# Optimization experiments

Measured on AMD Instinct MI355X. Metric: run time of the kernel, lower is better.

The kernel has to match this reference:

```python
import jax, jax.numpy as jnp
import numpy as np
from jax import lax

B, D, H, W = 1, 8, 64, 64
C, WS, NH = 192, 8, 6
N = WS ** 3          # 512 tokens per window
HD = C // NH         # 32
CONV_SCALE = 0.01
EPS = 1e-5
DN = ('NCDHW', 'OIDHW', 'NCDHW')


def _make_rpi():
    c = np.stack(np.meshgrid(np.arange(WS), np.arange(WS), np.arange(WS), indexing='ij')).reshape(3, -1)
    rel = (c[:, :, None] - c[:, None, :]).transpose(1, 2, 0) + (WS - 1)  # [N,N,3]
    idx = rel[..., 0] * (2 * WS - 1) ** 2 + rel[..., 1] * (2 * WS - 1) + rel[..., 2]
    return jnp.asarray(idx, dtype=jnp.int32)


def _ln(x, g, b):
    m = x.mean(-1, keepdims=True)
    v = jnp.mean((x - m) ** 2, -1, keepdims=True)
    return (x - m) * lax.rsqrt(v + EPS) * g + b


def setup_inputs() -> dict:
    key = jax.random.key(0)
    ks = jax.random.split(key, 16)
    s = 0.02
    inp = {
        'x': jax.random.normal(ks[0], (B, D * H * W, C), jnp.float32),
        'norm1_g': jnp.ones((C,), jnp.float32), 'norm1_b': jnp.zeros((C,), jnp.float32),
        'qkv_w': jax.random.normal(ks[1], (3 * C, C), jnp.float32) * s,
        'qkv_b': jnp.zeros((3 * C,), jnp.float32),
        'rpb_table': jax.random.normal(ks[2], (3375, NH), jnp.float32) * s,
        'proj_w': jax.random.normal(ks[3], (C, C), jnp.float32) * s,
        'proj_b': jnp.zeros((C,), jnp.float32),
        'conv1_w': jax.random.normal(ks[4], (C // 3, C, 3, 3, 3), jnp.float32) * s,
        'conv1_b': jnp.zeros((C // 3,), jnp.float32),
        'conv2_w': jax.random.normal(ks[5], (C, C // 3, 3, 3, 3), jnp.float32) * s,
        'conv2_b': jnp.zeros((C,), jnp.float32),
        'ca1_w': jax.random.normal(ks[6], (6, C), jnp.float32) * s,
        'ca1_b': jnp.zeros((6,), jnp.float32),
        'ca2_w': jax.random.normal(ks[7], (C, 6), jnp.float32) * s,
        'ca2_b': jnp.zeros((C,), jnp.float32),
        'norm2_g': jnp.ones((C,), jnp.float32), 'norm2_b': jnp.zeros((C,), jnp.float32),
        'fc1_w': jax.random.normal(ks[8], (4 * C, C), jnp.float32) * s,
        'fc1_b': jnp.zeros((4 * C,), jnp.float32),
        'fc2_w': jax.random.normal(ks[9], (C, 4 * C), jnp.float32) * s,
        'fc2_b': jnp.zeros((C,), jnp.float32),
        'rpi': _make_rpi(),
    }
    return inp


def reference(x, norm1_g, norm1_b, qkv_w, qkv_b, rpb_table, proj_w, proj_b,
              conv1_w, conv1_b, conv2_w, conv2_b, ca1_w, ca1_b, ca2_w, ca2_b,
              norm2_g, norm2_b, fc1_w, fc1_b, fc2_w, fc2_b, rpi):
    shortcut = x
    xn = _ln(x, norm1_g, norm1_b)                      # [B, L, C]
    x5 = xn.reshape(B, D, H, W, C)

    # ---- CAB3D conv branch (conv3x3 -> gelu -> conv3x3 -> channel attention)
    xc = jnp.transpose(x5, (0, 4, 1, 2, 3))            # NCDHW
    h = lax.conv_general_dilated(xc, conv1_w, (1, 1, 1), 'SAME', dimension_numbers=DN)
    h = jax.nn.gelu(h + conv1_b[None, :, None, None, None], approximate=False)
    h = lax.conv_general_dilated(h, conv2_w, (1, 1, 1), 'SAME', dimension_numbers=DN)
    h = h + conv2_b[None, :, None, None, None]
    pooled = h.mean(axis=(2, 3, 4))                    # [B, C] global avg pool
    a = jax.nn.relu(pooled @ ca1_w.T + ca1_b)
    a = jax.nn.sigmoid(a @ ca2_w.T + ca2_b)            # [B, C]
    conv_x = (h * a[:, :, None, None, None])
    conv_x = jnp.transpose(conv_x, (0, 2, 3, 4, 1)).reshape(B, D * H * W, C)

    # ---- window partition (shift_size forced to 0 since min(res)==window_size)
    xw = x5.reshape(B, D // WS, WS, H // WS, WS, W // WS, WS, C)
    xw = jnp.transpose(xw, (0, 1, 3, 5, 2, 4, 6, 7)).reshape(-1, N, C)  # [nW, N, C]

    # ---- window attention with relative position bias
    qkv = (xw @ qkv_w.T + qkv_b).reshape(-1, N, 3, NH, HD)
    q = jnp.transpose(qkv[:, :, 0], (0, 2, 1, 3)) * (HD ** -0.5)  # [nW, h, N, d]
    k = jnp.transpose(qkv[:, :, 1], (0, 2, 1, 3))
    v = jnp.transpose(qkv[:, :, 2], (0, 2, 1, 3))
    attn = jnp.einsum('whnd,whmd->whnm', q, k)
    bias = rpb_table[rpi]                              # [N, N, h]
    attn = attn + jnp.transpose(bias, (2, 0, 1))[None]
    attn = jax.nn.softmax(attn, axis=-1)
    out = jnp.einsum('whnm,whmd->whnd', attn, v)
    out = jnp.transpose(out, (0, 2, 1, 3)).reshape(-1, N, C)
    out = out @ proj_w.T + proj_b

    # ---- window reverse
    out = out.reshape(B, D // WS, H // WS, W // WS, WS, WS, WS, C)
    out = jnp.transpose(out, (0, 1, 4, 2, 5, 3, 6, 7)).reshape(B, D * H * W, C)

    x2 = shortcut + out + conv_x * CONV_SCALE
    xm = _ln(x2, norm2_g, norm2_b)
    xm = jax.nn.gelu(xm @ fc1_w.T + fc1_b, approximate=False) @ fc2_w.T + fc2_b
    return x2 + xm
```

## Files before the change

### kernel.cpp

```cpp
#include <hip/hip_runtime.h>
#include <hip/hip_bf16.h>

#define LTOK  32768
#define CDIM  192
#define DD_   8
#define HH_   64
#define WW_   64
#define NHEAD 6
#define HDIM  32
#define NWIN  64
#define NTOKW 512
#define C3    64
#define FCH   768

#define OFF_XN     0u
#define OFF_QH     6291456u
#define OFF_KH     9437184u
#define OFF_VH     12582912u
#define OFF_Y      15728640u
#define OFF_YBF    18874368u
#define OFF_H1     22020096u
#define OFF_H2     24117248u
#define OFF_PART   30408704u
#define OFF_AMASK  30457856u
#define OFF_BIAST  30458048u
#define OFF_W1T    32030912u
#define OFF_W2T    32362688u
#define OFF_QKVT   32694464u
#define OFF_PROJT  32805056u
#define OFF_FC1T   32841920u
#define OFF_FC2T   32989376u

typedef __attribute__((ext_vector_type(8)))  short short8v;
typedef __attribute__((ext_vector_type(16))) float f32x16;

union FragU { short8v v; unsigned u[4]; };

__device__ __forceinline__ float gelu_exact(float x) {
    return 0.5f * x * (1.0f + erff(x * 0.70710678118654752f));
}

__device__ __forceinline__ unsigned short bf16bits(float x) {
    union { __hip_bfloat16 b; unsigned short u; } cv;
    cv.b = __float2bfloat16(x);
    return cv.u;
}

__global__ __launch_bounds__(256) void k_ln(const float* __restrict__ in,
                                            const float* __restrict__ g,
                                            const float* __restrict__ b,
                                            float* __restrict__ out,
                                            __hip_bfloat16* __restrict__ obf) {
    int wv = threadIdx.x >> 6, lane = threadIdx.x & 63;
    int t = blockIdx.x * 4 + wv;
    const float* row = in + (size_t)t * CDIM;
    float x0 = row[lane], x1 = row[lane + 64], x2 = row[lane + 128];
    float s = x0 + x1 + x2;
    for (int o = 32; o; o >>= 1) s += __shfl_xor(s, o);
    float m = s * (1.0f / 192.0f);
    float d0 = x0 - m, d1 = x1 - m, d2 = x2 - m;
    float vv = d0 * d0 + d1 * d1 + d2 * d2;
    for (int o = 32; o; o >>= 1) vv += __shfl_xor(vv, o);
    float inv = rsqrtf(vv * (1.0f / 192.0f) + 1e-5f);
    size_t base = (size_t)t * CDIM;
    float y0 = d0 * inv * g[lane]       + b[lane];
    float y1 = d1 * inv * g[lane + 64]  + b[lane + 64];
    float y2 = d2 * inv * g[lane + 128] + b[lane + 128];
    if (out) {
        out[base + lane]       = y0;
        out[base + lane + 64]  = y1;
        out[base + lane + 128] = y2;
    }
    if (obf) {
        obf[base + lane]       = __float2bfloat16(y0);
        obf[base + lane + 64]  = __float2bfloat16(y1);
        obf[base + lane + 128] = __float2bfloat16(y2);
    }
}

__global__ void k_cast(const float* __restrict__ in, __hip_bfloat16* __restrict__ out, int n) {
    int i = blockIdx.x * 256 + threadIdx.x;
    if (i < n) out[i] = __float2bfloat16(in[i]);
}

__global__ void k_wp1(const float* __restrict__ w, __hip_bfloat16* __restrict__ wp) {
    int i = blockIdx.x * 256 + threadIdx.x;
    if (i >= 331776) return;
    int j = i & 7, oc = (i >> 3) & 63, h = (i >> 9) & 1;
    int cg = (i >> 10) % 12, kk = i / 12288;
    int c = cg * 16 + h * 8 + j;
    wp[i] = __float2bfloat16(w[((size_t)oc * 192 + c) * 27 + kk]);
}
__global__ void k_wp2(const float* __restrict__ w, __hip_bfloat16* __restrict__ wp) {
    int i = blockIdx.x * 256 + threadIdx.x;
    if (i >= 331776) return;
    int j = i & 7, oc = (i >> 3) % 192;
    int h = (i / 1536) & 1, cg = (i / 3072) & 3, kk = i / 12288;
    int c = cg * 16 + h * 8 + j;
    wp[i] = __float2bfloat16(w[((size_t)oc * 64 + c) * 27 + kk]);
}

__global__ __launch_bounds__(256) void k_bias(const int* __restrict__ rpi,
                                              const float* __restrict__ rpb,
                                              float* __restrict__ biasT) {
    __shared__ int idxl[64][64];
    int tid = threadIdx.x;
    int n0 = (blockIdx.x >> 3) * 64, m0 = (blockIdx.x & 7) * 64;
    for (int it = 0; it < 16; it++) {
        int e = it * 256 + tid;
        int ln_ = e >> 6, lm = e & 63;
        idxl[ln_][lm] = rpi[(size_t)(n0 + ln_) * NTOKW + m0 + lm];
    }
    __syncthreads();
    for (int it = 0; it < 16; it++) {
        int e = it * 256 + tid;
        int lm = e >> 6, ln_ = e & 63;
        int id = idxl[ln_][lm];
        #pragma unroll
        for (int h = 0; h < NHEAD; h++)
            biasT[(size_t)h * NTOKW * NTOKW + (size_t)(m0 + lm) * NTOKW + n0 + ln_] =
                rpb[id * NHEAD + h];
    }
}

__global__ __launch_bounds__(256) void k_conv1m(const __hip_bfloat16* __restrict__ xnbf,
                                                const __hip_bfloat16* __restrict__ w1p,
                                                const float* __restrict__ b1,
                                                __hip_bfloat16* __restrict__ h1bf) {
    __shared__ __align__(16) char lds[66 * 384];
    int tid = threadIdx.x;
    int wv = tid >> 6, lane = tid & 63;
    int wr = wv >> 1, wc = wv & 1;
    int half = lane >> 5, l31 = lane & 31;
    int row = blockIdx.x;
    int d = row >> 6, hh = row & 63;

    if (tid < 48) {
        float4 z = {0.f, 0.f, 0.f, 0.f};
        char* p = lds + ((tid < 24) ? tid * 16 : 65 * 384 + (tid - 24) * 16);
        *(float4*)p = z;
    }

    f32x16 acc;
    #pragma unroll
    for (int r = 0; r < 16; r++) acc[r] = 0.f;

    for (int kd = -1; kd <= 1; kd++) {
        int dd = d + kd;
        if (dd < 0 || dd >= DD_) continue;
        for (int kh = -1; kh <= 1; kh++) {
            int h2 = hh + kh;
            if (h2 < 0 || h2 >= HH_) continue;
            const short* src = (const short*)xnbf + ((size_t)((dd << 12) | (h2 << 6))) * CDIM;
            __syncthreads();
            #pragma unroll
            for (int it = 0; it < 6; it++) {
                int e16 = it * 256 + tid;
                int tok = e16 / 24, cb = (e16 % 24) * 16;
                short8v vdat = *(const short8v*)(src + e16 * 8);
                int lrow = tok + 1;
                *(short8v*)(lds + lrow * 384 + (cb ^ ((lrow & 7) << 4))) = vdat;
            }
            __syncthreads();
            #pragma unroll
            for (int kw = -1; kw <= 1; kw++) {
                int kk = (kd + 1) * 9 + (kh + 1) * 3 + (kw + 1);
                int atok = 32 * wr + l31 + kw + 1;
                int akey = (atok & 7) << 4;
                const char* abase = lds + atok * 384;
                const short* wbase = (const short*)w1p + (kk * 24 + half) * 512 + (32 * wc + l31) * 8;
                #pragma unroll
                for (int cg = 0; cg < 12; cg++) {
                    short8v af = *(const short8v*)(abase + ((cg * 32 + half * 16) ^ akey));
                    short8v bf = *(const short8v*)(wbase + cg * 1024);
                    acc = __builtin_amdgcn_mfma_f32_32x32x16_bf16(af, bf, acc, 0, 0, 0);
                }
            }
        }
    }
    int oc = 32 * wc + l31;
    float bb = b1[oc];
    int t0 = row * 64;
    #pragma unroll
    for (int r = 0; r < 16; r++) {
        int tok = 32 * wr + (r & 3) + 8 * (r >> 2) + 4 * half;
        h1bf[(size_t)(t0 + tok) * C3 + oc] = __float2bfloat16(gelu_exact(acc[r] + bb));
    }
}

__global__ __launch_bounds__(384) void k_conv2m(const __hip_bfloat16* __restrict__ h1bf,
                                                const __hip_bfloat16* __restrict__ w2p,
                                                const float* __restrict__ b2,
                                                float* __restrict__ h2) {
    __shared__ __align__(16) char lds[34 * 128];
    int tid = threadIdx.x;
    int wv = tid >> 6, lane = tid & 63;
    int half = lane >> 5, l31 = lane & 31;
    int row = blockIdx.x >> 1, hr = blockIdx.x & 1;
    int d = row >> 6, hh = row & 63;

    f32x16 acc;
    #pragma unroll
    for (int r = 0; r < 16; r++) acc[r] = 0.f;

    for (int kd = -1; kd <= 1; kd++) {
        int dd = d + kd;
        if (dd < 0 || dd >= DD_) continue;
        for (int kh = -1; kh <= 1; kh++) {
            int h2r = hh + kh;
            if (h2r < 0 || h2r >= HH_) continue;
            __syncthreads();
            if (tid < 272) {
                int ti = tid >> 3, cb = (tid & 7) * 16;
                int w = hr * 32 + ti - 1;
                short8v vdat = {0, 0, 0, 0, 0, 0, 0, 0};
                if (w >= 0 && w < 64)
                    vdat = *(const short8v*)((const short*)h1bf +
                           (size_t)((dd << 12) | (h2r << 6) | w) * C3 + cb / 2);
                *(short8v*)(lds + ti * 128 + (cb ^ ((ti & 7) << 4))) = vdat;
            }
            __syncthreads();
            #pragma unroll
            for (int kw = -1; kw <= 1; kw++) {
                int kk = (kd + 1) * 9 + (kh + 1) * 3 + (kw + 1);
                int atok = l31 + kw + 1;
                int akey = (atok & 7) << 4;
                const char* abase = lds + atok * 128;
                const short* wbase = (const short*)w2p + (kk * 8 + half) * 1536 + (wv * 32 + l31) * 8;
                #pragma unroll
                for (int cg = 0; cg < 4; cg++) {
                    short8v af = *(const short8v*)(abase + ((cg * 32 + half * 16) ^ akey));
                    short8v bf = *(const short8v*)(wbase + cg * 3072);
                    acc = __builtin_amdgcn_mfma_f32_32x32x16_bf16(af, bf, acc, 0, 0, 0);
                }
            }
        }
    }
    int oc = wv * 32 + l31;
    float bb = b2[oc];
    int t0 = row * 64 + hr * 32;
    #pragma unroll
    for (int r = 0; r < 16; r++) {
        int tok = (r & 3) + 8 * (r >> 2) + 4 * half;
        h2[(size_t)(t0 + tok) * CDIM + oc] = acc[r] + bb;
    }
}

__global__ __launch_bounds__(192) void k_pool(const float* __restrict__ h2,
                                              float* __restrict__ part) {
    int c = threadIdx.x, b = blockIdx.x;
    float s = 0.f;
    for (int i = 0; i < 128; i++) s += h2[(size_t)(b * 128 + i) * CDIM + c];
    part[b * CDIM + c] = s;
}

__global__ __launch_bounds__(192) void k_ca(const float* __restrict__ part,
                                            const float* __restrict__ ca1w,
                                            const float* __restrict__ ca1b,
                                            const float* __restrict__ ca2w,
                                            const float* __restrict__ ca2b,
                                            float* __restrict__ amask) {
    __shared__ float pooled[CDIM];
    __shared__ float hid[6];
    int c = threadIdx.x;
    float s = 0.f;
    for (int b = 0; b < 256; b++) s += part[b * CDIM + c];
    pooled[c] = s * (1.0f / 32768.0f);
    __syncthreads();
    if (c < 6) {
        float a = ca1b[c];
        for (int j = 0; j < CDIM; j++) a += ca1w[c * CDIM + j] * pooled[j];
        hid[c] = fmaxf(a, 0.f);
    }
    __syncthreads();
    float a = ca2b[c];
    for (int j = 0; j < 6; j++) a += ca2w[c * 6 + j] * hid[j];
    amask[c] = 1.0f / (1.0f + expf(-a));
}

__global__ __launch_bounds__(64) void k_qkvm(const __hip_bfloat16* __restrict__ xnbf,
                                             const __hip_bfloat16* __restrict__ qwb,
                                             const float* __restrict__ qkvb,
                                             __hip_bfloat16* __restrict__ q,
                                             __hip_bfloat16* __restrict__ k,
                                             __hip_bfloat16* __restrict__ v) {
    __shared__ __align__(16) char xlds[32 * 384];
    __shared__ float tb[32][33];
    int lane = threadIdx.x;
    int half = lane >> 5, l31 = lane & 31;
    int t0 = blockIdx.x * 32;
    int wi = t0 >> 9;
    int wh_ = wi >> 3, ww_ = wi & 7;

    #pragma unroll
    for (int it = 0; it < 12; it++) {
        int e16 = it * 64 + lane;
        int tok = e16 / 24, cb = (e16 % 24) * 16;
        int n = (t0 + tok) & 511;
        int nd = n >> 6, nh = (n >> 3) & 7, nw = n & 7;
        int torig = (nd << 12) | ((wh_ * 8 + nh) << 6) | (ww_ * 8 + nw);
        short8v vdat = *(const short8v*)((const short*)xnbf + (size_t)torig * CDIM + (e16 % 24) * 8);
        *(short8v*)(xlds + tok * 384 + (cb ^ ((tok & 7) << 4))) = vdat;
    }
    __syncthreads();

    int akey = (l31 & 7) << 4;
    const char* xbase = xlds + l31 * 384;

    for (int ti = 0; ti < 18; ti++) {
        f32x16 acc;
        #pragma unroll
        for (int r = 0; r < 16; r++) acc[r] = 0.f;
        const short* wbase = (const short*)qwb + (size_t)(ti * 32 + l31) * CDIM + half * 8;
        #pragma unroll
        for (int cg = 0; cg < 12; cg++) {
            short8v bf = *(const short8v*)(xbase + ((cg * 32 + half * 16) ^ akey));
            short8v af = *(const short8v*)(wbase + cg * 16);
            acc = __builtin_amdgcn_mfma_f32_32x32x16_bf16(af, bf, acc, 0, 0, 0);
        }
        #pragma unroll
        for (int r = 0; r < 16; r++) {
            int dl = (r & 3) + 8 * (r >> 2) + 4 * half;
            tb[l31][dl] = acc[r];
        }
        asm volatile("s_waitcnt lgkmcnt(0)" ::: "memory");
        __builtin_amdgcn_sched_barrier(0);
        int tok = lane >> 1, d0 = (lane & 1) * 16;
        int type = ti / 6, head = ti % 6;
        float scale = (type == 0) ? 0.17677669529663687f : 1.0f;
        int n = (t0 + tok) & 511;
        __hip_bfloat16* dst = (type == 0 ? q : (type == 1 ? k : v)) +
                              ((size_t)((wi * NHEAD + head) * NTOKW + n)) * HDIM + d0;
        const float* bp = qkvb + ti * 32 + d0;
        short8v o0, o1;
        #pragma unroll
        for (int i = 0; i < 8; i++)
            o0[i] = (short)bf16bits((tb[tok][d0 + i] + bp[i]) * scale);
        #pragma unroll
        for (int i = 0; i < 8; i++)
            o1[i] = (short)bf16bits((tb[tok][d0 + 8 + i] + bp[8 + i]) * scale);
        *(short8v*)((short*)dst) = o0;
        *(short8v*)((short*)dst + 8) = o1;
        asm volatile("s_waitcnt lgkmcnt(0)" ::: "memory");
        __builtin_amdgcn_sched_barrier(0);
    }
}

__global__ __launch_bounds__(256) void k_attn(const __hip_bfloat16* __restrict__ qh,
                                              const __hip_bfloat16* __restrict__ kh,
                                              const __hip_bfloat16* __restrict__ vh,
                                              const float* __restrict__ biasT,
                                              __hip_bfloat16* __restrict__ outbf) {
    __shared__ float ot[4][32][33];
    int wv = threadIdx.x >> 6, lane = threadIdx.x & 63;
    int tile = blockIdx.x * 4 + wv;
    int qt = tile & 15, wh = tile >> 4;
    int head = wh % NHEAD, wi = wh / NHEAD;
    int qb = qt * 32;
    int h = lane >> 5, ln31 = lane & 31;

    const unsigned short* qp = (const unsigned short*)qh + ((size_t)wh * NTOKW + qb + ln31) * HDIM;
    short8v qf0 = *(const short8v*)(qp + 8 * h);
    short8v qf1 = *(const short8v*)(qp + 16 + 8 * h);
    const unsigned short* kbase = (const unsigned short*)kh + (size_t)wh * NTOKW * HDIM;
    const unsigned short* vbase = (const unsigned short*)vh + (size_t)wh * NTOKW * HDIM;
    const float* bbase = biasT + (size_t)head * NTOKW * NTOKW + qb + ln31;

    f32x16 O;
    #pragma unroll
    for (int r = 0; r < 16; r++) O[r] = 0.f;
    float m = -1e30f, l = 0.f;

    for (int kb = 0; kb < NTOKW; kb += 32) {
        const unsigned short* kp = kbase + (size_t)(kb + ln31) * HDIM;
        short8v kf0 = *(const short8v*)(kp + 8 * h);
        short8v kf1 = *(const short8v*)(kp + 16 + 8 * h);
        f32x16 S;
        #pragma unroll
        for (int r = 0; r < 16; r++) S[r] = 0.f;
        S = __builtin_amdgcn_mfma_f32_32x32x16_bf16(kf0, qf0, S, 0, 0, 0);
        S = __builtin_amdgcn_mfma_f32_32x32x16_bf16(kf1, qf1, S, 0, 0, 0);

        float s[16];
        #pragma unroll
        for (int r = 0; r < 16; r++) {
            int key = (r & 3) + 8 * (r >> 2) + 4 * h;
            s[r] = S[r] + bbase[(size_t)(kb + key) * NTOKW];
        }
        float cm = s[0];
        #pragma unroll
        for (int r = 1; r < 16; r++) cm = fmaxf(cm, s[r]);
        cm = fmaxf(cm, __shfl_xor(cm, 32));
        float mn = fmaxf(m, cm);
        float scale = __expf(m - mn);
        float e[16]; float cs = 0.f;
        #pragma unroll
        for (int r = 0; r < 16; r++) { e[r] = __expf(s[r] - mn); cs += e[r]; }
        cs += __shfl_xor(cs, 32);
        l = l * scale + cs;
        m = mn;
        #pragma unroll
        for (int r = 0; r < 16; r++) O[r] *= scale;

        unsigned P[8], Qx[8];
        #pragma unroll
        for (int i = 0; i < 8; i++)
            P[i] = (unsigned)bf16bits(e[2 * i]) | ((unsigned)bf16bits(e[2 * i + 1]) << 16);
        #pragma unroll
        for (int i = 0; i < 8; i++) Qx[i] = __shfl_xor(P[i], 32);

        FragU p0, p1;
        p0.u[0] = h ? Qx[2] : P[0];  p0.u[1] = h ? Qx[3] : P[1];
        p0.u[2] = h ? P[2]  : Qx[0]; p0.u[3] = h ? P[3]  : Qx[1];
        p1.u[0] = h ? Qx[6] : P[4];  p1.u[1] = h ? Qx[7] : P[5];
        p1.u[2] = h ? P[6]  : Qx[4]; p1.u[3] = h ? P[7]  : Qx[5];

        const unsigned short* vp0 = vbase + (size_t)(kb + 8 * h) * HDIM + ln31;
        const unsigned short* vp1 = vbase + (size_t)(kb + 16 + 8 * h) * HDIM + ln31;
        short8v vf0, vf1;
        #pragma unroll
        for (int i = 0; i < 8; i++) {
            vf0[i] = (short)vp0[i * HDIM];
            vf1[i] = (short)vp1[i * HDIM];
        }
        O = __builtin_amdgcn_mfma_f32_32x32x16_bf16(vf0, p0.v, O, 0, 0, 0);
        O = __builtin_amdgcn_mfma_f32_32x32x16_bf16(vf1, p1.v, O, 0, 0, 0);
    }

    float invl = 1.0f / l;
    #pragma unroll
    for (int r = 0; r < 16; r++) {
        int d = (r & 3) + 8 * (r >> 2) + 4 * h;
        ot[wv][ln31][d] = O[r] * invl;
    }
    __syncthreads();
    int t2 = lane >> 1, c0 = (lane & 1) * 16;
    short* outp = (short*)outbf + ((size_t)(wi * NTOKW + qb + t2)) * CDIM + head * HDIM + c0;
    short8v s0, s1;
    #pragma unroll
    for (int i = 0; i < 8; i++) s0[i] = (short)bf16bits(ot[wv][t2][c0 + i]);
    #pragma unroll
    for (int i = 0; i < 8; i++) s1[i] = (short)bf16bits(ot[wv][t2][c0 + 8 + i]);
    *(short8v*)outp = s0;
    *(short8v*)(outp + 8) = s1;
}

__global__ __launch_bounds__(64) void k_projm(const __hip_bfloat16* __restrict__ attnbf,
                                              const __hip_bfloat16* __restrict__ pwb,
                                              const float* __restrict__ pb,
                                              const float* __restrict__ x,
                                              const float* __restrict__ h2,
                                              const float* __restrict__ amask,
                                              float* __restrict__ x2) {
    __shared__ __align__(16) char alds[32 * 384];
    __shared__ float tb[32][33];
    int lane = threadIdx.x;
    int half = lane >> 5, l31 = lane & 31;
    int t0 = blockIdx.x * 32;
    int wi = t0 >> 9;
    int wh_ = wi >> 3, ww_ = wi & 7;

    const short* src = (const short*)attnbf + (size_t)t0 * CDIM;
    #pragma unroll
    for (int it = 0; it < 12; it++) {
        int e16 = it * 64 + lane;
        int tok = e16 / 24, cb = (e16 % 24) * 16;
        short8v vdat = *(const short8v*)(src + e16 * 8);
        *(short8v*)(alds + tok * 384 + (cb ^ ((tok & 7) << 4))) = vdat;
    }
    __syncthreads();

    int akey = (l31 & 7) << 4;
    const char* abase = alds + l31 * 384;

    for (int ot = 0; ot < 6; ot++) {
        f32x16 acc;
        #pragma unroll
        for (int r = 0; r < 16; r++) acc[r] = 0.f;
        const short* wbase = (const short*)pwb + (size_t)(ot * 32 + l31) * CDIM + half * 8;
        #pragma unroll
        for (int cg = 0; cg < 12; cg++) {
            short8v bf = *(const short8v*)(abase + ((cg * 32 + half * 16) ^ akey));
            short8v af = *(const short8v*)(wbase + cg * 16);
            acc = __builtin_amdgcn_mfma_f32_32x32x16_bf16(af, bf, acc, 0, 0, 0);
        }
        #pragma unroll
        for (int r = 0; r < 16; r++) {
            int oc = (r & 3) + 8 * (r >> 2) + 4 * half;
            tb[l31][oc] = acc[r];
        }
        asm volatile("s_waitcnt lgkmcnt(0)" ::: "memory");
        __builtin_amdgcn_sched_barrier(0);
        int tok = lane >> 1, c0 = (lane & 1) * 16;
        int n = (t0 + tok) & 511;
        int nd = n >> 6, nh = (n >> 3) & 7, nw = n & 7;
        int t = (nd << 12) | ((wh_ * 8 + nh) << 6) | (ww_ * 8 + nw);
        size_t idx = (size_t)t * CDIM + ot * 32 + c0;
        const float* bp = pb + ot * 32 + c0;
        const float* ap = amask + ot * 32 + c0;
        #pragma unroll
        for (int i = 0; i < 16; i++)
            x2[idx + i] = x[idx + i] + tb[tok][c0 + i] + bp[i] + 0.01f * h2[idx + i] * ap[i];
        asm volatile("s_waitcnt lgkmcnt(0)" ::: "memory");
        __builtin_amdgcn_sched_barrier(0);
    }
}

__global__ __launch_bounds__(64) void k_mlpm(const __hip_bfloat16* __restrict__ ybf,
                                             const __hip_bfloat16* __restrict__ w1b,
                                             const float* __restrict__ b1,
                                             const __hip_bfloat16* __restrict__ w2b,
                                             const float* __restrict__ b2,
                                             float* __restrict__ out) {
    __shared__ __align__(16) char ylds[32 * 384];
    int lane = threadIdx.x;
    int half = lane >> 5, l31 = lane & 31;
    int t0 = blockIdx.x * 32;

    const short* src = (const short*)ybf + (size_t)t0 * CDIM;
    #pragma unroll
    for (int it = 0; it < 12; it++) {
        int e16 = it * 64 + lane;
        int tok = e16 / 24, cb = (e16 % 24) * 16;
        short8v vdat = *(const short8v*)(src + e16 * 8);
        *(short8v*)(ylds + tok * 384 + (cb ^ ((tok & 7) << 4))) = vdat;
    }
    __syncthreads();

    int akey = (l31 & 7) << 4;
    const char* ybase = ylds + l31 * 384;

    f32x16 oacc[6];
    #pragma unroll
    for (int ot = 0; ot < 6; ot++)
        #pragma unroll
        for (int r = 0; r < 16; r++) oacc[ot][r] = 0.f;

    for (int hc = 0; hc < 24; hc++) {
        f32x16 hacc;
        #pragma unroll
        for (int r = 0; r < 16; r++) hacc[r] = 0.f;
        const short* w1base = (const short*)w1b + (size_t)(hc * 32 + l31) * CDIM + half * 8;
        #pragma unroll
        for (int cg = 0; cg < 12; cg++) {
            short8v bf = *(const short8v*)(ybase + ((cg * 32 + half * 16) ^ akey));
            short8v af = *(const short8v*)(w1base + cg * 16);
            hacc = __builtin_amdgcn_mfma_f32_32x32x16_bf16(af, bf, hacc, 0, 0, 0);
        }
        float e[16];
        #pragma unroll
        for (int r = 0; r < 16; r++) {
            int hid = (r & 3) + 8 * (r >> 2) + 4 * half;
            e[r] = gelu_exact(hacc[r] + b1[hc * 32 + hid]);
        }
        unsigned P[8], Qx[8];
        #pragma unroll
        for (int i = 0; i < 8; i++)
            P[i] = (unsigned)bf16bits(e[2 * i]) | ((unsigned)bf16bits(e[2 * i + 1]) << 16);
        #pragma unroll
        for (int i = 0; i < 8; i++) Qx[i] = __shfl_xor(P[i], 32);
        FragU p0, p1;
        p0.u[0] = half ? Qx[2] : P[0];  p0.u[1] = half ? Qx[3] : P[1];
        p0.u[2] = half ? P[2]  : Qx[0]; p0.u[3] = half ? P[3]  : Qx[1];
        p1.u[0] = half ? Qx[6] : P[4];  p1.u[1] = half ? Qx[7] : P[5];
        p1.u[2] = half ? P[6]  : Qx[4]; p1.u[3] = half ? P[7]  : Qx[5];

        const short* w2base = (const short*)w2b + (size_t)l31 * FCH + hc * 32 + half * 8;
        #pragma unroll
        for (int ot = 0; ot < 6; ot++) {
            short8v a0 = *(const short8v*)(w2base + (size_t)ot * 32 * FCH);
            short8v a1 = *(const short8v*)(w2base + (size_t)ot * 32 * FCH + 16);
            oacc[ot] = __builtin_amdgcn_mfma_f32_32x32x16_bf16(a0, p0.v, oacc[ot], 0, 0, 0);
            oacc[ot] = __builtin_amdgcn_mfma_f32_32x32x16_bf16(a1, p1.v, oacc[ot], 0, 0, 0);
        }
    }

    __syncthreads();
    float* tbw = (float*)ylds;
    #pragma unroll
    for (int ot = 0; ot < 6; ot++) {
        #pragma unroll
        for (int r = 0; r < 16; r++) {
            int oc = (r & 3) + 8 * (r >> 2) + 4 * half;
            tbw[l31 * 33 + oc] = oacc[ot][r];
        }
        asm volatile("s_waitcnt lgkmcnt(0)" ::: "memory");
        __builtin_amdgcn_sched_barrier(0);
        int tok = lane >> 1, c0 = (lane & 1) * 16;
        float* op = out + (size_t)(t0 + tok) * CDIM + ot * 32 + c0;
        const float* bp = b2 + ot * 32 + c0;
        #pragma unroll
        for (int i = 0; i < 16; i++)
            op[i] += tbw[tok * 33 + c0 + i] + bp[i];
        asm volatile("s_waitcnt lgkmcnt(0)" ::: "memory");
        __builtin_amdgcn_sched_barrier(0);
    }
}

extern "C" void kernel_launch(void* const* d_in, const int* in_sizes, int n_in,
                              void* d_out, int out_size, void* d_ws, size_t ws_size,
                              hipStream_t stream) {
    const float* x     = (const float*)d_in[0];
    const float* n1g   = (const float*)d_in[1];
    const float* n1b   = (const float*)d_in[2];
    const float* qkvw  = (const float*)d_in[3];
    const float* qkvb  = (const float*)d_in[4];
    const float* rpb   = (const float*)d_in[5];
    const float* projw = (const float*)d_in[6];
    const float* projb = (const float*)d_in[7];
    const float* c1w   = (const float*)d_in[8];
    const float* c1b   = (const float*)d_in[9];
    const float* c2w   = (const float*)d_in[10];
    const float* c2b   = (const float*)d_in[11];
    const float* ca1w  = (const float*)d_in[12];
    const float* ca1b  = (const float*)d_in[13];
    const float* ca2w  = (const float*)d_in[14];
    const float* ca2b  = (const float*)d_in[15];
    const float* n2g   = (const float*)d_in[16];
    const float* n2b   = (const float*)d_in[17];
    const float* fc1w  = (const float*)d_in[18];
    const float* fc1b  = (const float*)d_in[19];
    const float* fc2w  = (const float*)d_in[20];
    const float* fc2b  = (const float*)d_in[21];
    const int*   rpi   = (const int*)d_in[22];

    float* ws  = (float*)d_ws;
    float* out = (float*)d_out;

    __hip_bfloat16* attnbf = (__hip_bfloat16*)(ws + OFF_XN);
    __hip_bfloat16* qh   = (__hip_bfloat16*)(ws + OFF_QH);
    __hip_bfloat16* kb_  = (__hip_bfloat16*)(ws + OFF_KH);
    __hip_bfloat16* vb_  = (__hip_bfloat16*)(ws + OFF_VH);
    __hip_bfloat16* xnbf = (__hip_bfloat16*)(ws + OFF_Y);
    __hip_bfloat16* ybf  = (__hip_bfloat16*)(ws + OFF_YBF);
    __hip_bfloat16* h1bf = (__hip_bfloat16*)(ws + OFF_H1);
    float* h2    = ws + OFF_H2;
    float* part  = ws + OFF_PART;
    float* amask = ws + OFF_AMASK;
    float* biasT = ws + OFF_BIAST;
    __hip_bfloat16* w1p  = (__hip_bfloat16*)(ws + OFF_W1T);
    __hip_bfloat16* w2p  = (__hip_bfloat16*)(ws + OFF_W2T);
    __hip_bfloat16* qwb  = (__hip_bfloat16*)(ws + OFF_QKVT);
    __hip_bfloat16* pwb  = (__hip_bfloat16*)(ws + OFF_PROJT);
    __hip_bfloat16* w1b  = (__hip_bfloat16*)(ws + OFF_FC1T);
    __hip_bfloat16* w2b  = (__hip_bfloat16*)(ws + OFF_FC2T);

    k_wp1<<<(331776 + 255) / 256, 256, 0, stream>>>(c1w, w1p);
    k_wp2<<<(331776 + 255) / 256, 256, 0, stream>>>(c2w, w2p);
    k_cast<<<(110592 + 255) / 256, 256, 0, stream>>>(qkvw, qwb, 110592);
    k_cast<<<(36864 + 255) / 256, 256, 0, stream>>>(projw, pwb, 36864);
    k_cast<<<(147456 + 255) / 256, 256, 0, stream>>>(fc1w, w1b, 147456);
    k_cast<<<(147456 + 255) / 256, 256, 0, stream>>>(fc2w, w2b, 147456);
    k_bias<<<64, 256, 0, stream>>>(rpi, rpb, biasT);

    k_ln<<<LTOK / 4, 256, 0, stream>>>(x, n1g, n1b, (float*)nullptr, xnbf);
    k_conv1m<<<512, 256, 0, stream>>>(xnbf, w1p, c1b, h1bf);
    k_conv2m<<<1024, 384, 0, stream>>>(h1bf, w2p, c2b, h2);
    k_pool<<<256, 192, 0, stream>>>(h2, part);
    k_ca<<<1, 192, 0, stream>>>(part, ca1w, ca1b, ca2w, ca2b, amask);
    k_qkvm<<<LTOK / 32, 64, 0, stream>>>(xnbf, qwb, qkvb, qh, kb_, vb_);
    k_attn<<<(NWIN * NHEAD * 16) / 4, 256, 0, stream>>>(qh, kb_, vb_, biasT, attnbf);
    k_projm<<<LTOK / 32, 64, 0, stream>>>(attnbf, pwb, projb, x, h2, amask, out);
    k_ln<<<LTOK / 4, 256, 0, stream>>>(out, n2g, n2b, (float*)nullptr, ybf);
    k_mlpm<<<LTOK / 32, 64, 0, stream>>>(ybf, w1b, fc1b, w2b, fc2b, out);
}
```

Measured before the change: 477.9 us.

## Split qkv, proj and MLP token-tile work across multiple waves per block

The QKV, projection and MLP GEMM kernels move from one wave per 32-token block to 3 or 4 waves that share the staged activation tile in LDS. In QKV each wave owns one of q/k/v, and in proj each wave owns two output column tiles. In the MLP kernel each wave handles a quarter of the hidden dimension, and the partial fc2 accumulators are summed through a swizzled LDS buffer in serialized wave order. The aim is more parallelism per block and less redundant LDS staging per wave. The cost is extra LDS, several barriers in the MLP reduction, and a serialized reduction step.

```diff
diff --git a/kernel.cpp b/kernel.cpp
--- a/kernel.cpp
+++ b/kernel.cpp
@@ -278,23 +278,24 @@
     amask[c] = 1.0f / (1.0f + expf(-a));
 }
 
-__global__ __launch_bounds__(64) void k_qkvm(const __hip_bfloat16* __restrict__ xnbf,
-                                             const __hip_bfloat16* __restrict__ qwb,
-                                             const float* __restrict__ qkvb,
-                                             __hip_bfloat16* __restrict__ q,
-                                             __hip_bfloat16* __restrict__ k,
-                                             __hip_bfloat16* __restrict__ v) {
+__global__ __launch_bounds__(192) void k_qkvm(const __hip_bfloat16* __restrict__ xnbf,
+                                              const __hip_bfloat16* __restrict__ qwb,
+                                              const float* __restrict__ qkvb,
+                                              __hip_bfloat16* __restrict__ q,
+                                              __hip_bfloat16* __restrict__ k,
+                                              __hip_bfloat16* __restrict__ v) {
     __shared__ __align__(16) char xlds[32 * 384];
-    __shared__ float tb[32][33];
-    int lane = threadIdx.x;
+    __shared__ float tb[3][32][33];
+    int tid = threadIdx.x;
+    int wv = tid >> 6, lane = tid & 63;
     int half = lane >> 5, l31 = lane & 31;
     int t0 = blockIdx.x * 32;
     int wi = t0 >> 9;
     int wh_ = wi >> 3, ww_ = wi & 7;
 
     #pragma unroll
-    for (int it = 0; it < 12; it++) {
-        int e16 = it * 64 + lane;
+    for (int it = 0; it < 4; it++) {
+        int e16 = it * 192 + tid;
         int tok = e16 / 24, cb = (e16 % 24) * 16;
         int n = (t0 + tok) & 511;
         int nd = n >> 6, nh = (n >> 3) & 7, nw = n & 7;
@@ -306,8 +307,11 @@
 
     int akey = (l31 & 7) << 4;
     const char* xbase = xlds + l31 * 384;
-
-    for (int ti = 0; ti < 18; ti++) {
+    __hip_bfloat16* dstbase = (wv == 0) ? q : (wv == 1 ? k : v);
+    float scale = (wv == 0) ? 0.17677669529663687f : 1.0f;
+
+    for (int j = 0; j < 6; j++) {
+        int ti = wv * 6 + j;
         f32x16 acc;
         #pragma unroll
         for (int r = 0; r < 16; r++) acc[r] = 0.f;
@@ -321,24 +325,22 @@
         #pragma unroll
         for (int r = 0; r < 16; r++) {
             int dl = (r & 3) + 8 * (r >> 2) + 4 * half;
-            tb[l31][dl] = acc[r];
+            tb[wv][l31][dl] = acc[r];
         }
         asm volatile("s_waitcnt lgkmcnt(0)" ::: "memory");
         __builtin_amdgcn_sched_barrier(0);
         int tok = lane >> 1, d0 = (lane & 1) * 16;
-        int type = ti / 6, head = ti % 6;
-        float scale = (type == 0) ? 0.17677669529663687f : 1.0f;
         int n = (t0 + tok) & 511;
-        __hip_bfloat16* dst = (type == 0 ? q : (type == 1 ? k : v)) +
-                              ((size_t)((wi * NHEAD + head) * NTOKW + n)) * HDIM + d0;
+        __hip_bfloat16* dst = dstbase +
+                              ((size_t)((wi * NHEAD + j) * NTOKW + n)) * HDIM + d0;
         const float* bp = qkvb + ti * 32 + d0;
         short8v o0, o1;
         #pragma unroll
         for (int i = 0; i < 8; i++)
-            o0[i] = (short)bf16bits((tb[tok][d0 + i] + bp[i]) * scale);
+            o0[i] = (short)bf16bits((tb[wv][tok][d0 + i] + bp[i]) * scale);
         #pragma unroll
         for (int i = 0; i < 8; i++)
-            o1[i] = (short)bf16bits((tb[tok][d0 + 8 + i] + bp[8 + i]) * scale);
+            o1[i] = (short)bf16bits((tb[wv][tok][d0 + 8 + i] + bp[8 + i]) * scale);
         *(short8v*)((short*)dst) = o0;
         *(short8v*)((short*)dst + 8) = o1;
         asm volatile("s_waitcnt lgkmcnt(0)" ::: "memory");
@@ -445,16 +447,17 @@
     *(short8v*)(outp + 8) = s1;
 }
 
-__global__ __launch_bounds__(64) void k_projm(const __hip_bfloat16* __restrict__ attnbf,
-                                              const __hip_bfloat16* __restrict__ pwb,
-                                              const float* __restrict__ pb,
-                                              const float* __restrict__ x,
-                                              const float* __restrict__ h2,
-                                              const float* __restrict__ amask,
-                                              float* __restrict__ x2) {
+__global__ __launch_bounds__(192) void k_projm(const __hip_bfloat16* __restrict__ attnbf,
+                                               const __hip_bfloat16* __restrict__ pwb,
+                                               const float* __restrict__ pb,
+                                               const float* __restrict__ x,
+                                               const float* __restrict__ h2,
+                                               const float* __restrict__ amask,
+                                               float* __restrict__ x2) {
     __shared__ __align__(16) char alds[32 * 384];
-    __shared__ float tb[32][33];
-    int lane = threadIdx.x;
+    __shared__ float tb[3][32][33];
+    int tid = threadIdx.x;
+    int wv = tid >> 6, lane = tid & 63;
     int half = lane >> 5, l31 = lane & 31;
     int t0 = blockIdx.x * 32;
     int wi = t0 >> 9;
@@ -462,8 +465,8 @@
 
     const short* src = (const short*)attnbf + (size_t)t0 * CDIM;
     #pragma unroll
-    for (int it = 0; it < 12; it++) {
-        int e16 = it * 64 + lane;
+    for (int it = 0; it < 4; it++) {
+        int e16 = it * 192 + tid;
         int tok = e16 / 24, cb = (e16 % 24) * 16;
         short8v vdat = *(const short8v*)(src + e16 * 8);
         *(short8v*)(alds + tok * 384 + (cb ^ ((tok & 7) << 4))) = vdat;
@@ -473,7 +476,8 @@
     int akey = (l31 & 7) << 4;
     const char* abase = alds + l31 * 384;
 
-    for (int ot = 0; ot < 6; ot++) {
+    for (int j = 0; j < 2; j++) {
+        int ot = wv * 2 + j;
         f32x16 acc;
         #pragma unroll
         for (int r = 0; r < 16; r++) acc[r] = 0.f;
@@ -487,7 +491,7 @@
         #pragma unroll
         for (int r = 0; r < 16; r++) {
             int oc = (r & 3) + 8 * (r >> 2) + 4 * half;
-            tb[l31][oc] = acc[r];
+            tb[wv][l31][oc] = acc[r];
         }
         asm volatile("s_waitcnt lgkmcnt(0)" ::: "memory");
         __builtin_amdgcn_sched_barrier(0);
@@ -500,27 +504,29 @@
         const float* ap = amask + ot * 32 + c0;
         #pragma unroll
         for (int i = 0; i < 16; i++)
-            x2[idx + i] = x[idx + i] + tb[tok][c0 + i] + bp[i] + 0.01f * h2[idx + i] * ap[i];
+            x2[idx + i] = x[idx + i] + tb[wv][tok][c0 + i] + bp[i] + 0.01f * h2[idx + i] * ap[i];
         asm volatile("s_waitcnt lgkmcnt(0)" ::: "memory");
         __builtin_amdgcn_sched_barrier(0);
     }
 }
 
-__global__ __launch_bounds__(64) void k_mlpm(const __hip_bfloat16* __restrict__ ybf,
-                                             const __hip_bfloat16* __restrict__ w1b,
-                                             const float* __restrict__ b1,
-                                             const __hip_bfloat16* __restrict__ w2b,
-                                             const float* __restrict__ b2,
-                                             float* __restrict__ out) {
+__global__ __launch_bounds__(256) void k_mlpm(const __hip_bfloat16* __restrict__ ybf,
+                                              const __hip_bfloat16* __restrict__ w1b,
+                                              const float* __restrict__ b1,
+                                              const __hip_bfloat16* __restrict__ w2b,
+                                              const float* __restrict__ b2,
+                                              float* __restrict__ out) {
     __shared__ __align__(16) char ylds[32 * 384];
-    int lane = threadIdx.x;
+    __shared__ __align__(16) float rbuf[6 * 32 * 32];
+    int tid = threadIdx.x;
+    int wv = tid >> 6, lane = tid & 63;
     int half = lane >> 5, l31 = lane & 31;
     int t0 = blockIdx.x * 32;
 
     const short* src = (const short*)ybf + (size_t)t0 * CDIM;
     #pragma unroll
-    for (int it = 0; it < 12; it++) {
-        int e16 = it * 64 + lane;
+    for (int it = 0; it < 3; it++) {
+        int e16 = it * 256 + tid;
         int tok = e16 / 24, cb = (e16 % 24) * 16;
         short8v vdat = *(const short8v*)(src + e16 * 8);
         *(short8v*)(ylds + tok * 384 + (cb ^ ((tok & 7) << 4))) = vdat;
@@ -536,7 +542,8 @@
         #pragma unroll
         for (int r = 0; r < 16; r++) oacc[ot][r] = 0.f;
 
-    for (int hc = 0; hc < 24; hc++) {
+    for (int j = 0; j < 6; j++) {
+        int hc = wv * 6 + j;
         f32x16 hacc;
         #pragma unroll
         for (int r = 0; r < 16; r++) hacc[r] = 0.f;
@@ -575,25 +582,42 @@
         }
     }
 
-    __syncthreads();
-    float* tbw = (float*)ylds;
-    #pragma unroll
-    for (int ot = 0; ot < 6; ot++) {
-        #pragma unroll
-        for (int r = 0; r < 16; r++) {
-            int oc = (r & 3) + 8 * (r >> 2) + 4 * half;
-            tbw[l31 * 33 + oc] = oacc[ot][r];
-        }
-        asm volatile("s_waitcnt lgkmcnt(0)" ::: "memory");
-        __builtin_amdgcn_sched_barrier(0);
-        int tok = lane >> 1, c0 = (lane & 1) * 16;
-        float* op = out + (size_t)(t0 + tok) * CDIM + ot * 32 + c0;
-        const float* bp = b2 + ot * 32 + c0;
-        #pragma unroll
-        for (int i = 0; i < 16; i++)
-            op[i] += tbw[tok * 33 + c0 + i] + bp[i];
-        asm volatile("s_waitcnt lgkmcnt(0)" ::: "memory");
-        __builtin_amdgcn_sched_barrier(0);
+    float4* rb4 = (float4*)rbuf;
+    for (int w = 0; w < 4; w++) {
+        if (wv == w) {
+            #pragma unroll
+            for (int ot = 0; ot < 6; ot++) {
+                #pragma unroll
+                for (int g = 0; g < 4; g++) {
+                    float4 val = {oacc[ot][g * 4 + 0], oacc[ot][g * 4 + 1],
+                                  oacc[ot][g * 4 + 2], oacc[ot][g * 4 + 3]};
+                    int chunk = 2 * g + half;
+                    float4* p = &rb4[(ot * 32 + l31) * 8 + (chunk ^ (l31 & 7))];
+                    if (w == 0) *p = val;
+                    else {
+                        float4 o = *p;
+                        o.x += val.x; o.y += val.y; o.z += val.z; o.w += val.w;
+                        *p = o;
+                    }
+                }
+            }
+        }
+        __syncthreads();
+    }
+
+    #pragma unroll
+    for (int i = 0; i < 6; i++) {
+        int c4 = i * 256 + tid;
+        int oc4 = c4 & 7;
+        int tok = (c4 >> 3) & 31;
+        int ot  = c4 >> 8;
+        float4 vv = rb4[(ot * 32 + tok) * 8 + (oc4 ^ (tok & 7))];
+        float* op = out + (size_t)(t0 + tok) * CDIM + ot * 32 + oc4 * 4;
+        const float* bp = b2 + ot * 32 + oc4 * 4;
+        op[0] += vv.x + bp[0];
+        op[1] += vv.y + bp[1];
+        op[2] += vv.z + bp[2];
+        op[3] += vv.w + bp[3];
     }
 }
 
@@ -658,9 +682,9 @@
     k_conv2m<<<1024, 384, 0, stream>>>(h1bf, w2p, c2b, h2);
     k_pool<<<256, 192, 0, stream>>>(h2, part);
     k_ca<<<1, 192, 0, stream>>>(part, ca1w, ca1b, ca2w, ca2b, amask);
-    k_qkvm<<<LTOK / 32, 64, 0, stream>>>(xnbf, qwb, qkvb, qh, kb_, vb_);
+    k_qkvm<<<LTOK / 32, 192, 0, stream>>>(xnbf, qwb, qkvb, qh, kb_, vb_);
     k_attn<<<(NWIN * NHEAD * 16) / 4, 256, 0, stream>>>(qh, kb_, vb_, biasT, attnbf);
-    k_projm<<<LTOK / 32, 64, 0, stream>>>(attnbf, pwb, projb, x, h2, amask, out);
+    k_projm<<<LTOK / 32, 192, 0, stream>>>(attnbf, pwb, projb, x, h2, amask, out);
     k_ln<<<LTOK / 4, 256, 0, stream>>>(out, n2g, n2b, (float*)nullptr, ybf);
-    k_mlpm<<<LTOK / 32, 64, 0, stream>>>(ybf, w1b, fc1b, w2b, fc2b, out);
-}
+    k_mlpm<<<LTOK / 32, 256, 0, stream>>>(ybf, w1b, fc1b, w2b, fc2b, out);
+}
```

After: 430.2 us. -10.0%, faster.
